# Performance work log

Measured on AMD Instinct MI355X. Metric: run time of the kernel, lower is better.

## Reference

```python
import jax, jax.numpy as jnp
import numpy as np

B, S, DIN, D, H, L, M, C = 64, 800, 64, 512, 8, 2, 64, 2
DH = D // H          # head dim = 64
FF = 4 * D           # feedforward hidden = 2048
EPS_K = 1e-4         # performer softmax-kernel epsilon
LN_EPS = 1e-5


def setup_inputs() -> dict:
    rng = np.random.default_rng(0)
    def w(*shape, scale=0.02):
        return jnp.asarray(rng.normal(0.0, scale, shape).astype(np.float32))
    def ortho_proj():
        # gaussian orthogonal random matrix (FAVOR+), one DHxDH block since M == DH
        blk = rng.normal(size=(DH, DH))
        q, _ = np.linalg.qr(blk)
        mult = np.linalg.norm(rng.normal(size=(M, DH)), axis=1)
        return (mult[:, None] * q.T).astype(np.float32)
    proj = jnp.asarray(np.stack([ortho_proj() for _ in range(L)]))  # [L,M,DH]
    zeros = lambda *s: jnp.zeros(s, jnp.float32)
    ones = lambda *s: jnp.ones(s, jnp.float32)
    return {
        'x': w(B, S, DIN, scale=1.0),
        'emb_w': w(DIN, D), 'emb_b': zeros(D),
        'pos': w(1, S, D, scale=1.0),
        'ln1_g': ones(L, D), 'ln1_b': zeros(L, D),
        'wq': w(L, D, D), 'bq': zeros(L, D),
        'wk': w(L, D, D), 'bk': zeros(L, D),
        'wv': w(L, D, D), 'bv': zeros(L, D),
        'wo': w(L, D, D), 'bo': zeros(L, D),
        'proj': proj,
        'ln2_g': ones(L, D), 'ln2_b': zeros(L, D),
        'w1': w(L, D, FF), 'b1': zeros(L, FF),
        'w2': w(L, FF, D), 'b2': zeros(L, D),
        'fc_w': w(D, C), 'fc_b': zeros(C),
    }


def _ln(x, g, b):
    m = x.mean(-1, keepdims=True)
    v = jnp.var(x, axis=-1, keepdims=True)
    return (x - m) * jax.lax.rsqrt(v + LN_EPS) * g + b


def _softmax_kernel(data, proj, is_query):
    # data [B,H,S,DH], proj [M,DH] -> positive random features [B,H,S,M]
    norm = 1.0 / np.sqrt(np.sqrt(DH))
    ratio = 1.0 / np.sqrt(M)
    dn = data * norm
    dd = jnp.einsum('bhsd,md->bhsm', dn, proj)
    diag = 0.5 * jnp.sum(dn * dn, axis=-1, keepdims=True)  # [B,H,S,1]
    if is_query:
        stab = jax.lax.stop_gradient(jnp.max(dd, axis=-1, keepdims=True))
    else:
        stab = jax.lax.stop_gradient(jnp.max(dd, axis=(-2, -1), keepdims=True))
    return ratio * (jnp.exp(dd - diag - stab) + EPS_K)


def _heads(t):
    return t.reshape(B, S, H, DH).transpose(0, 2, 1, 3)  # [B,H,S,DH]


def _forward(x, emb_w, emb_b, pos, ln1_g, ln1_b, wq, bq, wk, bk, wv, bv, wo, bo,
             proj, ln2_g, ln2_b, w1, b1, w2, b2, fc_w, fc_b):
    h = x @ emb_w + emb_b + pos[:, :S]
    for l in range(L):
        # FAVOR+ attention block (pre-LN, residual)
        y = _ln(h, ln1_g[l], ln1_b[l])
        q = _heads(y @ wq[l] + bq[l])
        k = _heads(y @ wk[l] + bk[l])
        v = _heads(y @ wv[l] + bv[l])
        qp = _softmax_kernel(q, proj[l], True)   # [B,H,S,M]
        kp = _softmax_kernel(k, proj[l], False)  # [B,H,S,M]
        ctx = jnp.einsum('bhsm,bhsd->bhmd', kp, v)        # [B,H,M,DH]
        out = jnp.einsum('bhsm,bhmd->bhsd', qp, ctx)      # [B,H,S,DH]
        d_inv = 1.0 / jnp.einsum('bhsm,bhm->bhs', qp, kp.sum(axis=2))
        out = (out * d_inv[..., None]).transpose(0, 2, 1, 3).reshape(B, S, D)
        h = h + out @ wo[l] + bo[l]
        # FFN block (pre-LN, residual)
        y = _ln(h, ln2_g[l], ln2_b[l])
        h = h + jax.nn.gelu(y @ w1[l] + b1[l]) @ w2[l] + b2[l]
    return h.mean(axis=1) @ fc_w + fc_b  # [B,C]


def reference(x, emb_w, emb_b, pos, ln1_g, ln1_b, wq, bq, wk, bk, wv, bv, wo, bo,
              proj, ln2_g, ln2_b, w1, b1, w2, b2, fc_w, fc_b):
    return _forward(x, emb_w, emb_b, pos, ln1_g, ln1_b, wq, bq, wk, bk, wv, bv,
                    wo, bo, proj, ln2_g, ln2_b, w1, b1, w2, b2, fc_w, fc_b)
```

## Files before the change

kernel.cpp:

```cpp
#include <hip/hip_runtime.h>
#include <hip/hip_bf16.h>

#define B_   64
#define S_   800
#define DIN_ 64
#define D_   512
#define H_   8
#define DH_  64
#define M_   64
#define L_   2
#define FF_  2048

typedef __hip_bfloat16 bf16;
typedef __attribute__((ext_vector_type(8))) short bf16x8;
typedef __attribute__((ext_vector_type(4))) float f32x4;
typedef __attribute__((ext_vector_type(2))) float f32x2;

#define NORM_ 0.35355339059327373f

__device__ __forceinline__ float bf2f(unsigned short s){
  return __uint_as_float(((unsigned)s)<<16);
}
__device__ __forceinline__ float gelu_f(float x){
  float u = 0.7978845608028654f*(x + 0.044715f*x*x*x);
  float e = __expf(2.f*u);
  float t = 1.f - 2.f/(1.f + e);
  return 0.5f*x*(1.f + t);
}
__device__ __forceinline__ void st_bf4(bf16* p, float4 v){
  union { bf16 b[4]; unsigned long long u; } q;
  q.b[0]=__float2bfloat16(v.x); q.b[1]=__float2bfloat16(v.y);
  q.b[2]=__float2bfloat16(v.z); q.b[3]=__float2bfloat16(v.w);
  *(unsigned long long*)p = q.u;
}
__device__ __forceinline__ void gld16(const void* g, void* l){
  __builtin_amdgcn_global_load_lds((const __attribute__((address_space(1))) void*)g,
                                   (__attribute__((address_space(3))) void*)l, 16, 0, 0);
}

__device__ __forceinline__ void swz_xy(int gx, int& bx, int& by){
  const int nwg = (int)gridDim.x, orig = (int)blockIdx.x;
  const int q = nwg>>3, r = nwg&7;
  const int xcd = orig&7, lin = orig>>3;
  const int wg = (xcd<r ? xcd*(q+1) : r*(q+1)+(xcd-r)*q) + lin;
  bx = wg % gx;  by = wg / gx;
}

__device__ __forceinline__ void gemm_tile256(const bf16* __restrict__ A,
                                             const bf16* __restrict__ Wt,
                                             int rows, int K, int bx, int by,
                                             f32x4 (&acc)[8][4])
{
  __shared__ bf16 As[2][16384];
  __shared__ bf16 Bs[2][16384];
  const int tid = threadIdx.x, wave = tid>>6, lane = tid&63;
  const int wr = wave>>2, wc = wave&3;
  const int lr = lane&15, hi = lane>>4;
  const int row0 = by*256, col0 = bx*256;
  const int srow = tid>>3;
  const int scol = ((tid&7) ^ ((srow>>1)&7))*8;
  const int keyq = (lr>>1)&7;
  const bf16* gA[4]; const bf16* gB[4];
  #pragma unroll
  for (int i=0;i<4;i++){
    const int ra = min(row0 + i*64 + srow, rows-1);
    gA[i] = A  + (size_t)ra*K + scol;
    gB[i] = Wt + (size_t)(col0 + i*64 + srow)*K + scol;
  }
  const int dbase = wave*512;
  const int NT = K>>6;
  #pragma unroll
  for (int i=0;i<4;i++){
    gld16(gA[i], &As[0][i*4096 + dbase]);
    gld16(gB[i], &Bs[0][i*4096 + dbase]);
  }
  __syncthreads();
  for (int t=0; t<NT; ++t){
    const int p = t&1;
    if (t+1 < NT){
      const int k0 = (t+1)<<6;
      #pragma unroll
      for (int i=0;i<4;i++){
        gld16(gA[i] + k0, &As[p^1][i*4096 + dbase]);
        gld16(gB[i] + k0, &Bs[p^1][i*4096 + dbase]);
      }
    }
    #pragma unroll
    for (int ks=0; ks<2; ++ks){
      const int co = ((ks*4 + hi) ^ keyq)*8;
      bf16x8 af[8], bv[4];
      #pragma unroll
      for (int mi=0;mi<8;mi++)
        af[mi] = *(const bf16x8*)&As[p][(wr*128 + mi*16 + lr)*64 + co];
      #pragma unroll
      for (int ni=0;ni<4;ni++)
        bv[ni] = *(const bf16x8*)&Bs[p][(wc*64 + ni*16 + lr)*64 + co];
      #pragma unroll
      for (int mi=0;mi<8;mi++)
        #pragma unroll
        for (int ni=0;ni<4;ni++)
          acc[mi][ni] = __builtin_amdgcn_mfma_f32_16x16x32_bf16(af[mi], bv[ni], acc[mi][ni], 0,0,0);
    }
    __syncthreads();
  }
}

template<int ACT, int RES, int OUTB>
__global__ __launch_bounds__(512,2)
void gemm256_k(const bf16* __restrict__ A, const bf16* __restrict__ Wt,
               const float* __restrict__ bias, const bf16* __restrict__ res,
               float* __restrict__ Cf, bf16* __restrict__ Cb,
               int rows, int N, int K, int gx)
{
  int bx, by;  swz_xy(gx, bx, by);
  f32x4 acc[8][4];
  #pragma unroll
  for (int i=0;i<8;i++)
    #pragma unroll
    for (int j=0;j<4;j++) acc[i][j] = (f32x4){0.f,0.f,0.f,0.f};
  gemm_tile256(A, Wt, rows, K, bx, by, acc);
  const int tid=threadIdx.x, wave=tid>>6, lane=tid&63;
  const int wr=wave>>2, wc=wave&3, lr=lane&15, hi=lane>>4;
  const int row0=by*256, col0=bx*256;
  #pragma unroll
  for (int mi=0;mi<8;mi++){
    #pragma unroll
    for (int i=0;i<4;i++){
      const int r = row0 + wr*128 + mi*16 + hi*4 + i;
      if (r >= rows) continue;
      #pragma unroll
      for (int ni=0;ni<4;ni++){
        const int c = col0 + wc*64 + ni*16 + lr;
        float v = acc[mi][ni][i] + bias[c];
        if (ACT) v = gelu_f(v);
        if (RES) v += bf2f(*(const unsigned short*)&res[(size_t)r*N + c]);
        if (OUTB) Cb[(size_t)r*N + c] = __float2bfloat16(v);
        else      Cf[(size_t)r*N + c] = v;
      }
    }
  }
}

__global__ __launch_bounds__(512,1)
void mega256_k(const bf16* __restrict__ A, const bf16* __restrict__ Wcat,
               const float* __restrict__ bcat, const float* __restrict__ invm2,
               int rows,
               bf16* __restrict__ qpb, bf16* __restrict__ ddk,
               bf16* __restrict__ vbf, int gx)
{
  int bx, by;  swz_xy(gx, bx, by);
  f32x4 acc[8][4];
  #pragma unroll
  for (int i=0;i<8;i++)
    #pragma unroll
    for (int j=0;j<4;j++) acc[i][j] = (f32x4){0.f,0.f,0.f,0.f};
  gemm_tile256(A, Wcat, rows, 512, bx, by, acc);
  const int tid=threadIdx.x, wave=tid>>6, lane=tid&63;
  const int wr=wave>>2, wc=wave&3, lr=lane&15, hi=lane>>4;
  const int row0 = by*256;
  const int cbase = bx*256 + wc*64;
  float bb[4];
  #pragma unroll
  for (int ni=0;ni<4;ni++) bb[ni] = bcat[cbase + ni*16 + lr];

  if (bx < 4){
    const int isK = bx>>1;
    const int h = (bx&1)*4 + wc;
    float im[4];
    #pragma unroll
    for (int ni=0;ni<4;ni++) im[ni] = invm2[ni*16 + lr];
    float ds[32];
    #pragma unroll
    for (int mi=0;mi<8;mi++)
      #pragma unroll
      for (int i=0;i<4;i++){
        float v0=acc[mi][0][i]+bb[0], v1=acc[mi][1][i]+bb[1];
        float v2=acc[mi][2][i]+bb[2], v3=acc[mi][3][i]+bb[3];
        ds[mi*4+i] = v0*v0*im[0] + v1*v1*im[1] + v2*v2*im[2] + v3*v3*im[3];
      }
    #pragma unroll
    for (int st=1; st<=8; st<<=1)
      #pragma unroll
      for (int idx=0;idx<32;idx++) ds[idx] += __shfl_xor(ds[idx], st);
    #pragma unroll
    for (int mi=0;mi<8;mi++){
      #pragma unroll
      for (int i=0;i<4;i++){
        const int r = row0 + wr*128 + mi*16 + hi*4 + i;
        if (r >= rows) continue;
        const float dg = 0.5f*ds[mi*4+i];
        if (!isK){
          #pragma unroll
          for (int ni=0;ni<4;ni++)
            qpb[(size_t)r*512 + h*64 + ni*16 + lr] =
                __float2bfloat16(0.125f*(__expf(acc[mi][ni][i]+bb[ni] - dg) + 1e-4f));
        } else {
          #pragma unroll
          for (int ni=0;ni<4;ni++)
            ddk[(size_t)r*512 + h*64 + ni*16 + lr] =
                __float2bfloat16(acc[mi][ni][i]+bb[ni] - dg);
        }
      }
    }
  } else {
    const int colb = (bx-4)*256 + wc*64;
    #pragma unroll
    for (int mi=0;mi<8;mi++){
      #pragma unroll
      for (int i=0;i<4;i++){
        const int r = row0 + wr*128 + mi*16 + hi*4 + i;
        if (r >= rows) continue;
        #pragma unroll
        for (int ni=0;ni<4;ni++)
          vbf[(size_t)r*512 + colb + ni*16 + lr] =
              __float2bfloat16(acc[mi][ni][i] + bb[ni]);
      }
    }
  }
}

__device__ __forceinline__ void gemm_tile(const bf16* __restrict__ A,
                                          const bf16* __restrict__ Wt,
                                          int rows, int K, int bx, int by,
                                          f32x4 (&acc)[4][4])
{
  __shared__ bf16 As[3*4096];
  __shared__ bf16 Bs[3*4096];
  const int tid = threadIdx.x, wave = tid>>6, lane = tid&63;
  const int row0 = by*128, col0 = bx*128;
  const int wm = (wave>>1)*64, wn = (wave&1)*64;
  const int lr = lane&15;
  const int lk = ((lane>>4) ^ ((lane>>1)&3))*8;
  const int c0 = wave*2, c1 = c0+1;
  const int sub = lane>>2;
  const int kq = (((lane&3) ^ ((lane>>3)&3)))*8;
  const int ra0 = min(row0 + c0*16 + sub, rows-1);
  const int ra1 = min(row0 + c1*16 + sub, rows-1);
  const bf16* gA0 = A + (size_t)ra0*K + kq;
  const bf16* gA1 = A + (size_t)ra1*K + kq;
  const bf16* gB0 = Wt + (size_t)(col0 + c0*16 + sub)*K + kq;
  const bf16* gB1 = Wt + (size_t)(col0 + c1*16 + sub)*K + kq;
  const int o0 = c0*512, o1 = c1*512;
  const int nt = K>>5;
  gld16(gA0, &As[o0]);  gld16(gA1, &As[o1]);
  gld16(gB0, &Bs[o0]);  gld16(gB1, &Bs[o1]);
  __syncthreads();
  int cur = 0;
  for (int t=0; t<nt; ++t){
    const int nxt = (cur+4096 > 8192) ? 0 : cur+4096;
    if (t+1 < nt){
      const int k0 = (t+1)*32;
      gld16(gA0+k0, &As[nxt+o0]);  gld16(gA1+k0, &As[nxt+o1]);
      gld16(gB0+k0, &Bs[nxt+o0]);  gld16(gB1+k0, &Bs[nxt+o1]);
    }
    bf16x8 af[4], bv[4];
    #pragma unroll
    for (int mi=0;mi<4;mi++) af[mi] = *(const bf16x8*)&As[cur + (wm+mi*16+lr)*32 + lk];
    #pragma unroll
    for (int ni=0;ni<4;ni++) bv[ni] = *(const bf16x8*)&Bs[cur + (wn+ni*16+lr)*32 + lk];
    #pragma unroll
    for (int mi=0;mi<4;mi++)
      #pragma unroll
      for (int ni=0;ni<4;ni++)
        acc[mi][ni] = __builtin_amdgcn_mfma_f32_16x16x32_bf16(af[mi], bv[ni], acc[mi][ni], 0,0,0);
    __syncthreads();
    cur = nxt;
  }
}

template<int ACT, int RES, int OUTB>
__global__ __launch_bounds__(256)
void gemm2_k(const bf16* __restrict__ A, const bf16* __restrict__ Wt,
             const float* __restrict__ bias, const bf16* __restrict__ res,
             float* __restrict__ Cf, bf16* __restrict__ Cb,
             int rows, int N, int K, int res_mod, int gx)
{
  int bx, by;  swz_xy(gx, bx, by);
  f32x4 acc[4][4];
  #pragma unroll
  for (int i=0;i<4;i++)
    #pragma unroll
    for (int j=0;j<4;j++) acc[i][j] = (f32x4){0.f,0.f,0.f,0.f};
  gemm_tile(A, Wt, rows, K, bx, by, acc);
  const int tid=threadIdx.x, wave=tid>>6, lane=tid&63;
  const int wm=(wave>>1)*64, wn=(wave&1)*64, lr=lane&15, hi=lane>>4;
  const int row0=by*128, col0=bx*128;
  #pragma unroll
  for (int mi=0;mi<4;mi++){
    #pragma unroll
    for (int i=0;i<4;i++){
      const int r = row0 + wm + mi*16 + hi*4 + i;
      if (r >= rows) continue;
      #pragma unroll
      for (int ni=0;ni<4;ni++){
        const int c = col0 + wn + ni*16 + lr;
        float v = acc[mi][ni][i] + bias[c];
        if (ACT) v = gelu_f(v);
        if (RES) v += bf2f(*(const unsigned short*)&res[(size_t)(res_mod ? (r % res_mod) : r)*N + c]);
        if (OUTB) Cb[(size_t)r*N + c] = __float2bfloat16(v);
        else      Cf[(size_t)r*N + c] = v;
      }
    }
  }
}

__global__ __launch_bounds__(256)
void convT_k(const float* __restrict__ src, bf16* __restrict__ dst, int K, int N,
             int mapbase, int mapstride)
{
  __shared__ float t[32][33];
  const int n0 = blockIdx.x*32, k0 = blockIdx.y*32;
  const int j = threadIdx.x&31, i0 = threadIdx.x>>5;
  #pragma unroll
  for (int i=i0; i<32; i+=8) t[i][j] = src[(size_t)(k0+i)*N + n0 + j];
  __syncthreads();
  #pragma unroll
  for (int i=i0; i<32; i+=8){
    const int n = n0 + i;
    const int rn = mapbase + (n>>6)*mapstride + (n&63);
    dst[(size_t)rn*K + k0 + j] = __float2bfloat16(t[j][i]);
  }
}

__global__ void conv_k(const float* __restrict__ src, bf16* __restrict__ dst, int n4)
{
  int i = blockIdx.x*256 + threadIdx.x;
  if (i < n4){ float4 v = ((const float4*)src)[i]; st_bf4(dst + (size_t)i*4, v); }
}

__global__ __launch_bounds__(256)
void projw_k(const float* __restrict__ w, const float* __restrict__ proj,
             bf16* __restrict__ Wcat, int mapbase)
{
  __shared__ float pj[64][64];
  __shared__ float wsh[64][65];
  const int h = blockIdx.x, c0 = blockIdx.y*64;
  const int tid = threadIdx.x, lane = tid&63, tg = tid>>6;
  for (int i=tid; i<4096; i+=256) pj[i>>6][i&63] = proj[i];
  for (int i=tg; i<64; i+=4) wsh[i][lane] = w[(size_t)(c0+i)*512 + h*64 + lane];
  __syncthreads();
  float acc[16];
  #pragma unroll
  for (int j=0;j<16;j++) acc[j]=0.f;
  for (int d=0; d<64; ++d){
    float wv = wsh[lane][d];
    #pragma unroll
    for (int j=0;j<16;j++) acc[j] += wv * pj[tg*16+j][d];
  }
  #pragma unroll
  for (int j=0;j<16;j++)
    Wcat[(size_t)(mapbase + h*64 + tg*16 + j)*512 + c0 + lane] = __float2bfloat16(acc[j]*NORM_);
}

__global__ void bpack_k(const float* __restrict__ bq, const float* __restrict__ bk,
                        const float* __restrict__ bv, const float* __restrict__ proj,
                        float* __restrict__ bl)
{
  int idx = blockIdx.x*256 + threadIdx.x;
  if (idx >= 1536) return;
  float v;
  if (idx < 1024){
    const float* bsrc = (idx<512)? bq : bk;
    int t = idx & 511;
    int h = t>>6, m = t&63;
    float acc=0.f;
    for (int d=0; d<64; ++d) acc += bsrc[h*64+d]*proj[m*64+d];
    v = acc*NORM_;
  } else v = bv[idx-1024];
  bl[idx] = v;
}

__global__ void invm_k(const float* __restrict__ proj, float* __restrict__ invm2)
{
  int m = threadIdx.x;
  if (m < 64){
    float s = 0.f;
    for (int d=0; d<64; ++d){ float p = proj[m*64+d]; s += p*p; }
    invm2[m] = 1.f/s;
  }
}

__global__ __launch_bounds__(256)
void ln_k(const bf16* __restrict__ x, const float* __restrict__ g,
          const float* __restrict__ b, bf16* __restrict__ y, int nrows)
{
  const int wid = threadIdx.x>>6, lane = threadIdx.x&63;
  float gv[8], bv[8];
  {
    float4 t0 = *(const float4*)(g + lane*8);
    float4 t1 = *(const float4*)(g + lane*8 + 4);
    gv[0]=t0.x;gv[1]=t0.y;gv[2]=t0.z;gv[3]=t0.w;gv[4]=t1.x;gv[5]=t1.y;gv[6]=t1.z;gv[7]=t1.w;
    float4 u0 = *(const float4*)(b + lane*8);
    float4 u1 = *(const float4*)(b + lane*8 + 4);
    bv[0]=u0.x;bv[1]=u0.y;bv[2]=u0.z;bv[3]=u0.w;bv[4]=u1.x;bv[5]=u1.y;bv[6]=u1.z;bv[7]=u1.w;
  }
  for (size_t row = (size_t)blockIdx.x*4 + wid; row < (size_t)nrows; row += (size_t)gridDim.x*4){
    bf16x8 xv = *(const bf16x8*)(x + row*D_ + lane*8);
    float f[8];
    #pragma unroll
    for (int j=0;j<8;j++) f[j] = bf2f((unsigned short)xv[j]);
    float s=0.f, ss=0.f;
    #pragma unroll
    for (int j=0;j<8;j++){ s += f[j]; ss += f[j]*f[j]; }
    #pragma unroll
    for (int o=32;o;o>>=1){ s += __shfl_xor(s,o); ss += __shfl_xor(ss,o); }
    const float mean = s*(1.f/D_);
    const float rstd = rsqrtf(ss*(1.f/D_) - mean*mean + 1e-5f);
    union { bf16 bb[8]; bf16x8 v8; } o8;
    #pragma unroll
    for (int j=0;j<8;j++)
      o8.bb[j] = __float2bfloat16((f[j]-mean)*rstd*gv[j] + bv[j]);
    *(bf16x8*)(y + row*D_ + lane*8) = o8.v8;
  }
}

__global__ __launch_bounds__(256)
void fctx_k(const bf16* __restrict__ ddk, const bf16* __restrict__ vbf,
            float* __restrict__ ctx, float* __restrict__ kps)
{
  __shared__ float kc[32][64], vc[32][64];
  const int bh = blockIdx.x, tid = threadIdx.x;
  const int b = bh>>3, h = bh&7;
  const int mq = tid>>4, dq = tid&15;
  const int cc = (tid&15)*4;
  f32x2 acc2[2][4];
  #pragma unroll
  for (int p=0;p<2;p++)
    #pragma unroll
    for (int j=0;j<4;j++) acc2[p][j] = (f32x2){0.f,0.f};
  float kpart[4] = {0.f,0.f,0.f,0.f};
  for (int s0=0; s0<S_; s0+=32){
    #pragma unroll
    for (int ii=0; ii<2; ++ii){
      const int rr = (tid>>4) + ii*16;
      const size_t grow = (size_t)(b*S_+s0+rr)*512 + h*64 + cc;
      ushort4 du = *(const ushort4*)(ddk + grow);
      float4 kv;
      kv.x = 0.125f*(__expf(bf2f(du.x))+1e-4f);
      kv.y = 0.125f*(__expf(bf2f(du.y))+1e-4f);
      kv.z = 0.125f*(__expf(bf2f(du.z))+1e-4f);
      kv.w = 0.125f*(__expf(bf2f(du.w))+1e-4f);
      *(float4*)&kc[rr][cc] = kv;
      kpart[0]+=kv.x; kpart[1]+=kv.y; kpart[2]+=kv.z; kpart[3]+=kv.w;
      ushort4 vu = *(const ushort4*)(vbf + grow);
      float4 vv;
      vv.x = bf2f(vu.x); vv.y = bf2f(vu.y);
      vv.z = bf2f(vu.z); vv.w = bf2f(vu.w);
      *(float4*)&vc[rr][cc] = vv;
    }
    __syncthreads();
    #pragma unroll 8
    for (int ssi=0; ssi<32; ++ssi){
      f32x2 a0 = *(const f32x2*)&kc[ssi][mq*4 + 0];
      f32x2 a1 = *(const f32x2*)&kc[ssi][mq*4 + 2];
      float4 b4 = *(const float4*)&vc[ssi][dq*4];
      acc2[0][0] += a0 * (f32x2){b4.x,b4.x};
      acc2[0][1] += a0 * (f32x2){b4.y,b4.y};
      acc2[0][2] += a0 * (f32x2){b4.z,b4.z};
      acc2[0][3] += a0 * (f32x2){b4.w,b4.w};
      acc2[1][0] += a1 * (f32x2){b4.x,b4.x};
      acc2[1][1] += a1 * (f32x2){b4.y,b4.y};
      acc2[1][2] += a1 * (f32x2){b4.z,b4.z};
      acc2[1][3] += a1 * (f32x2){b4.w,b4.w};
    }
    __syncthreads();
  }
  #pragma unroll
  for (int p=0;p<2;p++)
    #pragma unroll
    for (int j=0;j<4;j++){
      ctx[((size_t)bh*64 + mq*4 + 2*p    )*64 + dq*4+j] = acc2[p][j].x;
      ctx[((size_t)bh*64 + mq*4 + 2*p + 1)*64 + dq*4+j] = acc2[p][j].y;
    }
  float* kcf = &kc[0][0];
  #pragma unroll
  for (int j=0;j<4;j++) kcf[tid*4+j] = kpart[j];
  __syncthreads();
  if (tid < 64){
    const int m = tid;
    float s = 0.f;
    #pragma unroll
    for (int g=0; g<16; ++g) s += kcf[(g*16 + (m>>2))*4 + (m&3)];
    kps[bh*64 + m] = s;
  }
}

__global__ __launch_bounds__(256)
void attnout_k(const bf16* __restrict__ qpb, const float* __restrict__ ctx,
               const float* __restrict__ kps, bf16* __restrict__ out)
{
  __shared__ float cl[4096];
  __shared__ float kl[64];
  __shared__ float qL[4][64];
  const int bh = blockIdx.x, tid = threadIdx.x;
  for (int i=tid;i<4096;i+=256) cl[i] = ctx[(size_t)bh*4096 + i];
  if (tid<64) kl[tid] = kps[bh*64+tid];
  __syncthreads();
  const int b = bh>>3, h = bh&7;
  const int d = tid&63, sg = tid>>6;
  const int send = min((int)(blockIdx.y*64+64), S_);
  for (int s0 = blockIdx.y*64; s0 < send; s0 += 4){
    const int sr = s0 + sg;
    const size_t rrow = (size_t)(b*S_+sr);
    float qp = bf2f(*(const unsigned short*)&qpb[rrow*512 + h*64 + d]);
    qL[sg][d] = qp;
    float a0=0,a1=0,a2=0,a3=0, e0=0,e1=0,e2=0,e3=0;
    #pragma unroll
    for (int m=0;m<64;m+=4){
      float q0=qL[sg][m], q1=qL[sg][m+1], q2=qL[sg][m+2], q3=qL[sg][m+3];
      a0 += q0*cl[(m  )*64+d]; a1 += q1*cl[(m+1)*64+d];
      a2 += q2*cl[(m+2)*64+d]; a3 += q3*cl[(m+3)*64+d];
      e0 += q0*kl[m]; e1 += q1*kl[m+1]; e2 += q2*kl[m+2]; e3 += q3*kl[m+3];
    }
    const float den = (e0+e1)+(e2+e3);
    const float o = ((a0+a1)+(a2+a3))/den;
    out[(rrow*H_ + h)*64 + d] = __float2bfloat16(o);
  }
}

__global__ __launch_bounds__(256)
void head_k(const bf16* __restrict__ h, const float* __restrict__ fcw,
            const float* __restrict__ fcb, float* __restrict__ out)
{
  __shared__ float red[256][2];
  const int b = blockIdx.x, tid = threadIdx.x;
  const bf16* hb = h + (size_t)b*S_*D_;
  float s0=0.f, s1=0.f;
  for (int s=0; s<S_; ++s){
    s0 += bf2f(*(const unsigned short*)&hb[(size_t)s*D_ + tid]);
    s1 += bf2f(*(const unsigned short*)&hb[(size_t)s*D_ + tid + 256]);
  }
  const float m0 = s0*(1.f/S_), m1 = s1*(1.f/S_);
  red[tid][0] = m0*fcw[tid*2+0] + m1*fcw[(tid+256)*2+0];
  red[tid][1] = m0*fcw[tid*2+1] + m1*fcw[(tid+256)*2+1];
  __syncthreads();
  for (int st=128; st; st>>=1){
    if (tid<st){ red[tid][0]+=red[tid+st][0]; red[tid][1]+=red[tid+st][1]; }
    __syncthreads();
  }
  if (tid==0){ out[b*2+0]=red[0][0]+fcb[0]; out[b*2+1]=red[0][1]+fcb[1]; }
}

extern "C" void kernel_launch(void* const* d_in, const int* in_sizes, int n_in,
                              void* d_out, int out_size, void* d_ws, size_t ws_size,
                              hipStream_t stream)
{
  const float* x     = (const float*)d_in[0];
  const float* emb_w = (const float*)d_in[1];
  const float* emb_b = (const float*)d_in[2];
  const float* pos   = (const float*)d_in[3];
  const float* ln1_g = (const float*)d_in[4];
  const float* ln1_b = (const float*)d_in[5];
  const float* wq    = (const float*)d_in[6];
  const float* bq    = (const float*)d_in[7];
  const float* wk    = (const float*)d_in[8];
  const float* bk    = (const float*)d_in[9];
  const float* wv    = (const float*)d_in[10];
  const float* bv    = (const float*)d_in[11];
  const float* wo    = (const float*)d_in[12];
  const float* bo    = (const float*)d_in[13];
  const float* proj  = (const float*)d_in[14];
  const float* ln2_g = (const float*)d_in[15];
  const float* ln2_b = (const float*)d_in[16];
  const float* w1    = (const float*)d_in[17];
  const float* b1    = (const float*)d_in[18];
  const float* w2    = (const float*)d_in[19];
  const float* b2    = (const float*)d_in[20];
  const float* fc_w  = (const float*)d_in[21];
  const float* fc_b  = (const float*)d_in[22];
  float* out = (float*)d_out;

  const size_t W55 = (size_t)512*512, W52 = (size_t)512*2048;
  const size_t WCAT = (size_t)1536*512;

  char* p = (char*)d_ws;
  auto take = [&](size_t bytes)->char*{
    char* r = p; p += (bytes + 255) & ~(size_t)255; return r;
  };
  bf16* Wcat = (bf16*)take(L_*WCAT*2);
  bf16* woT  = (bf16*)take(L_*W55*2);
  bf16* w1T  = (bf16*)take(L_*W52*2);
  bf16* w2T  = (bf16*)take(L_*W52*2);
  bf16* embT = (bf16*)take((size_t)64*512*2);
  bf16* xbf  = (bf16*)take((size_t)B_*S_*DIN_*2);
  bf16* posbf= (bf16*)take((size_t)S_*512*2);
  float* bcat= (float*)take(L_*1536*4);
  float* invm= (float*)take(L_*64*4);
  const size_t fixed_bytes = (size_t)(p - (char*)d_ws);

  int NB = 32; size_t need = 0;
  for (;; NB >>= 1){
    size_t RC = (size_t)NB*S_, nbh = (size_t)NB*H_;
    need = fixed_bytes + RC*(5*1024 + 4096) + nbh*(16384+256) + 65536;
    if (need <= ws_size || NB == 1) break;
  }
  if (need > ws_size) return;
  const size_t RC = (size_t)NB*S_;
  const int NBH = NB*H_, rows = (int)RC;

  bf16*  hbuf = (bf16*)take(RC*512*2);
  bf16*  qpb  = (bf16*)take(RC*512*2);
  bf16*  ddk  = (bf16*)take(RC*512*2);
  bf16*  vbf  = (bf16*)take(RC*512*2);
  bf16*  ybf  = (bf16*)take(RC*512*2);
  bf16*  hidbf= (bf16*)take(RC*2048*2);
  float* ctx  = (float*)take((size_t)NBH*4096*4);
  float* kps  = (float*)take((size_t)NBH*64*4);

  dim3 blk(256), blk5(512);

  for (int l=0; l<L_; ++l){
    bf16* Wl = Wcat + (size_t)l*WCAT;
    float* bl = bcat + (size_t)l*1536;
    projw_k<<<dim3(8,8),   blk, 0, stream>>>(wq + l*W55, proj + l*4096, Wl, 0);
    projw_k<<<dim3(8,8),   blk, 0, stream>>>(wk + l*W55, proj + l*4096, Wl, 512);
    convT_k<<<dim3(16,16), blk, 0, stream>>>(wv + l*W55, Wl, 512, 512, 1024, 64);
    bpack_k<<<6, blk, 0, stream>>>(bq + l*512, bk + l*512, bv + l*512, proj + l*4096, bl);
    invm_k<<<1, 64, 0, stream>>>(proj + l*4096, invm + l*64);
    convT_k<<<dim3(16,16), blk, 0, stream>>>(wo + l*W55, woT + l*W55, 512, 512, 0, 64);
    convT_k<<<dim3(64,16), blk, 0, stream>>>(w1 + l*W52, w1T + l*W52, 512, 2048, 0, 64);
    convT_k<<<dim3(16,64), blk, 0, stream>>>(w2 + l*W52, w2T + l*W52, 2048, 512, 0, 64);
  }
  convT_k<<<dim3(16,2), blk, 0, stream>>>(emb_w, embT, 64, 512, 0, 64);
  conv_k<<<(B_*S_*DIN_/4 + 255)/256, blk, 0, stream>>>(x, xbf, B_*S_*DIN_/4);
  conv_k<<<(S_*512/4 + 255)/256, blk, 0, stream>>>(pos, posbf, S_*512/4);

  const int rg128 = (rows + 127)/128;
  const int rg256 = (rows + 255)/256;

  for (int bc = 0; bc < B_/NB; ++bc){
    const bf16* xc = xbf + (size_t)bc*RC*DIN_;
    float* outc = out + (size_t)bc*NB*2;

    gemm2_k<0,1,1><<<4*rg128, blk, 0, stream>>>(
        xc, embT, emb_b, posbf, nullptr, hbuf, rows, 512, 64, S_, 4);

    for (int l=0; l<L_; ++l){
      ln_k<<<2048, blk, 0, stream>>>(hbuf, ln1_g + l*512, ln1_b + l*512, ybf, rows);
      mega256_k<<<6*rg256, blk5, 0, stream>>>(
          ybf, Wcat + (size_t)l*WCAT, bcat + (size_t)l*1536, invm + l*64, rows,
          qpb, ddk, vbf, 6);
      fctx_k<<<NBH, blk, 0, stream>>>(ddk, vbf, ctx, kps);
      attnout_k<<<dim3(NBH, (S_+63)/64), blk, 0, stream>>>(qpb, ctx, kps, ybf);
      gemm256_k<0,1,1><<<2*rg256, blk5, 0, stream>>>(
          ybf, woT + l*W55, bo + l*512, hbuf, nullptr, hbuf, rows, 512, 512, 2);
      ln_k<<<2048, blk, 0, stream>>>(hbuf, ln2_g + l*512, ln2_b + l*512, ybf, rows);
      gemm256_k<1,0,1><<<8*rg256, blk5, 0, stream>>>(
          ybf, w1T + l*W52, b1 + l*2048, nullptr, nullptr, hidbf, rows, 2048, 512, 8);
      gemm256_k<0,1,1><<<2*rg256, blk5, 0, stream>>>(
          hidbf, w2T + l*W52, b2 + l*512, hbuf, nullptr, hbuf, rows, 512, 2048, 2);
    }
    head_k<<<NB, blk, 0, stream>>>(hbuf, fc_w, fc_b, outc);
  }
}
```

Measured before the change: 1.999 ms.

## Compute attention output with bf16 MFMA and fold denominator as extra column

Replaces the scalar FP32 attention-output kernel with an MFMA-based kernel. It stores ctx transposed in bf16 and appends the key-feature sum as an extra B-matrix row, so the normalising denominator comes out of the same matrix multiply. Shared memory uses an XOR swizzle to avoid bank conflicts, and each block now covers 256 sequence rows instead of 64. In exchange, ctx and kps are rounded to bf16, which lowers precision in the numerator and denominator.

```diff
diff --git a/kernel.cpp b/kernel.cpp
--- a/kernel.cpp
+++ b/kernel.cpp
@@ -416,7 +416,7 @@
 
 __global__ __launch_bounds__(256)
 void fctx_k(const bf16* __restrict__ ddk, const bf16* __restrict__ vbf,
-            float* __restrict__ ctx, float* __restrict__ kps)
+            bf16* __restrict__ ctxT, float* __restrict__ kps)
 {
   __shared__ float kc[32][64], vc[32][64];
   const int bh = blockIdx.x, tid = threadIdx.x;
@@ -469,8 +469,9 @@
   for (int p=0;p<2;p++)
     #pragma unroll
     for (int j=0;j<4;j++){
-      ctx[((size_t)bh*64 + mq*4 + 2*p    )*64 + dq*4+j] = acc2[p][j].x;
-      ctx[((size_t)bh*64 + mq*4 + 2*p + 1)*64 + dq*4+j] = acc2[p][j].y;
+      const int d = dq*4 + j;
+      ctxT[(size_t)bh*4096 + d*64 + mq*4 + 2*p    ] = __float2bfloat16(acc2[p][j].x);
+      ctxT[(size_t)bh*4096 + d*64 + mq*4 + 2*p + 1] = __float2bfloat16(acc2[p][j].y);
     }
   float* kcf = &kc[0][0];
   #pragma unroll
@@ -486,35 +487,70 @@
 }
 
 __global__ __launch_bounds__(256)
-void attnout_k(const bf16* __restrict__ qpb, const float* __restrict__ ctx,
-               const float* __restrict__ kps, bf16* __restrict__ out)
-{
-  __shared__ float cl[4096];
-  __shared__ float kl[64];
-  __shared__ float qL[4][64];
+void attnmm_k(const bf16* __restrict__ qpb, const bf16* __restrict__ ctxT,
+              const float* __restrict__ kps, bf16* __restrict__ out)
+{
+  __shared__ bf16 Bs[80*64];
   const int bh = blockIdx.x, tid = threadIdx.x;
-  for (int i=tid;i<4096;i+=256) cl[i] = ctx[(size_t)bh*4096 + i];
-  if (tid<64) kl[tid] = kps[bh*64+tid];
+  const int b = bh>>3, h = bh&7;
+  for (int idx=tid; idx<640; idx+=256){
+    const int row = idx>>3, q = idx&7;
+    const int sq = q ^ ((row>>1)&7);
+    bf16x8 v;
+    if (row < 64){
+      v = *(const bf16x8*)(ctxT + (size_t)bh*4096 + row*64 + sq*8);
+    } else if (row == 64){
+      const float* kp = kps + bh*64 + sq*8;
+      union { bf16 bb[8]; bf16x8 v8; } u;
+      #pragma unroll
+      for (int j=0;j<8;j++) u.bb[j] = __float2bfloat16(kp[j]);
+      v = u.v8;
+    } else {
+      v = (bf16x8){0,0,0,0,0,0,0,0};
+    }
+    *(bf16x8*)(&Bs[row*64 + q*8]) = v;
+  }
   __syncthreads();
-  const int b = bh>>3, h = bh&7;
-  const int d = tid&63, sg = tid>>6;
-  const int send = min((int)(blockIdx.y*64+64), S_);
-  for (int s0 = blockIdx.y*64; s0 < send; s0 += 4){
-    const int sr = s0 + sg;
-    const size_t rrow = (size_t)(b*S_+sr);
-    float qp = bf2f(*(const unsigned short*)&qpb[rrow*512 + h*64 + d]);
-    qL[sg][d] = qp;
-    float a0=0,a1=0,a2=0,a3=0, e0=0,e1=0,e2=0,e3=0;
-    #pragma unroll
-    for (int m=0;m<64;m+=4){
-      float q0=qL[sg][m], q1=qL[sg][m+1], q2=qL[sg][m+2], q3=qL[sg][m+3];
-      a0 += q0*cl[(m  )*64+d]; a1 += q1*cl[(m+1)*64+d];
-      a2 += q2*cl[(m+2)*64+d]; a3 += q3*cl[(m+3)*64+d];
-      e0 += q0*kl[m]; e1 += q1*kl[m+1]; e2 += q2*kl[m+2]; e3 += q3*kl[m+3];
-    }
-    const float den = (e0+e1)+(e2+e3);
-    const float o = ((a0+a1)+(a2+a3))/den;
-    out[(rrow*H_ + h)*64 + d] = __float2bfloat16(o);
+  const int wave = tid>>6, lane = tid&63;
+  const int lr = lane&15, hi = lane>>4;
+  const int s0 = blockIdx.y*256 + wave*64;
+  const int keyq = (lr>>1)&7;
+  f32x4 acc[4][5];
+  #pragma unroll
+  for (int i=0;i<4;i++)
+    #pragma unroll
+    for (int j=0;j<5;j++) acc[i][j] = (f32x4){0.f,0.f,0.f,0.f};
+  #pragma unroll
+  for (int ks=0; ks<2; ++ks){
+    bf16x8 af[4], bv[5];
+    #pragma unroll
+    for (int mi=0;mi<4;mi++){
+      const int s = min(s0 + mi*16 + lr, S_-1);
+      af[mi] = *(const bf16x8*)(qpb + (size_t)(b*S_+s)*512 + h*64 + ks*32 + hi*8);
+    }
+    #pragma unroll
+    for (int ni=0;ni<5;ni++)
+      bv[ni] = *(const bf16x8*)&Bs[(ni*16+lr)*64 + ((ks*4+hi)^keyq)*8];
+    #pragma unroll
+    for (int mi=0;mi<4;mi++)
+      #pragma unroll
+      for (int ni=0;ni<5;ni++)
+        acc[mi][ni] = __builtin_amdgcn_mfma_f32_16x16x32_bf16(af[mi], bv[ni], acc[mi][ni], 0,0,0);
+  }
+  #pragma unroll
+  for (int mi=0;mi<4;mi++){
+    #pragma unroll
+    for (int i=0;i<4;i++){
+      const float den = __shfl(acc[mi][4][i], (lane & 48));
+      const float inv = 1.f/den;
+      const int s = s0 + mi*16 + hi*4 + i;
+      if (s >= S_) continue;
+      const size_t rrow = (size_t)(b*S_+s);
+      #pragma unroll
+      for (int ni=0;ni<4;ni++)
+        out[(rrow*H_ + h)*64 + ni*16 + lr] =
+            __float2bfloat16(acc[mi][ni][i] * inv);
+    }
   }
 }
 
@@ -591,7 +627,7 @@
   int NB = 32; size_t need = 0;
   for (;; NB >>= 1){
     size_t RC = (size_t)NB*S_, nbh = (size_t)NB*H_;
-    need = fixed_bytes + RC*(5*1024 + 4096) + nbh*(16384+256) + 65536;
+    need = fixed_bytes + RC*(5*1024 + 4096) + nbh*(8192+256) + 65536;
     if (need <= ws_size || NB == 1) break;
   }
   if (need > ws_size) return;
@@ -604,7 +640,7 @@
   bf16*  vbf  = (bf16*)take(RC*512*2);
   bf16*  ybf  = (bf16*)take(RC*512*2);
   bf16*  hidbf= (bf16*)take(RC*2048*2);
-  float* ctx  = (float*)take((size_t)NBH*4096*4);
+  bf16*  ctxT = (bf16*)take((size_t)NBH*4096*2);
   float* kps  = (float*)take((size_t)NBH*64*4);
 
   dim3 blk(256), blk5(512);
@@ -640,8 +676,8 @@
       mega256_k<<<6*rg256, blk5, 0, stream>>>(
           ybf, Wcat + (size_t)l*WCAT, bcat + (size_t)l*1536, invm + l*64, rows,
           qpb, ddk, vbf, 6);
-      fctx_k<<<NBH, blk, 0, stream>>>(ddk, vbf, ctx, kps);
-      attnout_k<<<dim3(NBH, (S_+63)/64), blk, 0, stream>>>(qpb, ctx, kps, ybf);
+      fctx_k<<<NBH, blk, 0, stream>>>(ddk, vbf, ctxT, kps);
+      attnmm_k<<<dim3(NBH, (S_+255)/256), blk, 0, stream>>>(qpb, ctxT, kps, ybf);
       gemm256_k<0,1,1><<<2*rg256, blk5, 0, stream>>>(
           ybf, woT + l*W55, bo + l*512, hbuf, nullptr, hbuf, rows, 512, 512, 2);
       ln_k<<<2048, blk, 0, stream>>>(hbuf, ln2_g + l*512, ln2_b + l*512, ybf, rows);
```

Result: faster. 1.675 ms (-16.2%).
